# Performance work log

Hardware: AMD Instinct MI355X
Metric: run time of the kernel (lower is better)

The kernel has to match this reference:

```python
import jax, jax.numpy as jnp
import numpy as np

N, L, D, H, DFF = 16, 192, 512, 8, 2048
HD = D // H


def _mha(q, k, v, wq, bq, wk, bk, wv, bv, wo, bo, mask=None):
    # q: [B, Lq, D], k/v: [B, Lk, D]
    B, Lq, _ = q.shape
    def proj(x, W, b):
        y = x @ W + b
        return y.reshape(B, -1, H, HD).transpose(0, 2, 1, 3)  # [B, H, L, HD]
    Q, K, V = proj(q, wq, bq), proj(k, wk, bk), proj(v, wv, bv)
    QK = jnp.einsum('bhqd,bhkd->bhqk', Q, K) / jnp.sqrt(jnp.asarray(HD, Q.dtype))
    if mask is not None:
        QK = QK + (1.0 - mask) * (-1e9)
    A = jax.nn.softmax(QK, axis=-1)
    out = jnp.einsum('bhqk,bhkd->bhqd', A, V).transpose(0, 2, 1, 3).reshape(B, Lq, D)
    return out @ wo + bo


def _ln(x, g, b, eps=1e-6):
    mu = x.mean(-1, keepdims=True)
    var = ((x - mu) ** 2).mean(-1, keepdims=True)
    return (x - mu) / jnp.sqrt(var + eps) * g + b


def setup_inputs() -> dict:
    key = jax.random.key(0)
    ks = jax.random.split(key, 16)
    w = lambda k, sh: jax.random.normal(k, sh, jnp.float32) * 0.02
    inp = {
        'S': jax.random.normal(ks[0], (N, L, D), jnp.float32),
        'padding_mask': jax.random.randint(ks[1], (N * N, 1, 1, L), 0, 2, dtype=jnp.int32),
        'training': 0,
    }
    for i, nm in enumerate(['ca_wq', 'ca_wk', 'ca_wv', 'ca_wo', 'ia_wq', 'ia_wk', 'ia_wv', 'ia_wo']):
        inp[nm] = w(ks[2 + i], (D, D))
        inp[nm.replace('w', 'b')] = jnp.zeros((D,), jnp.float32)
    inp['ffn_w1'] = w(ks[10], (D, DFF)); inp['ffn_b1'] = jnp.zeros((DFF,), jnp.float32)
    inp['ffn_w2'] = w(ks[11], (DFF, D)); inp['ffn_b2'] = jnp.zeros((D,), jnp.float32)
    inp['ln1_g'] = jnp.ones((D,), jnp.float32); inp['ln1_b'] = jnp.zeros((D,), jnp.float32)
    inp['ln2_g'] = jnp.ones((D,), jnp.float32); inp['ln2_b'] = jnp.zeros((D,), jnp.float32)
    return inp


def reference(S, ca_wq, ca_bq, ca_wk, ca_bk, ca_wv, ca_bv, ca_wo, ca_bo,
              ia_wq, ia_bq, ia_wk, ia_bk, ia_wv, ia_bv, ia_wo, ia_bo,
              ffn_w1, ffn_b1, ffn_w2, ffn_b2, ln1_g, ln1_b, ln2_g, ln2_b,
              padding_mask, training):
    # training == 0 -> dropout layers are identity (inference mode)
    mask = padding_mask.astype(S.dtype)
    n, l, d = S.shape
    # all-pairs cross attention: query seq i attends to key/value seq j
    queries = jnp.repeat(S, n, axis=0)   # [n*n, l, d]
    keyvalue = jnp.tile(S, (n, 1, 1))    # [n*n, l, d]
    S_attn = _mha(queries, keyvalue, keyvalue,
                  ca_wq, ca_bq, ca_wk, ca_bk, ca_wv, ca_bv, ca_wo, ca_bo, mask=mask)
    S_attn = S_attn.reshape(n, n, l, d).transpose(1, 2, 0, 3).reshape(n * l, n, d)
    S_flip = S.reshape(n * l, 1, d)
    S_attn = _mha(S_flip, S_attn, S_attn,
                  ia_wq, ia_bq, ia_wk, ia_bk, ia_wv, ia_bv, ia_wo, ia_bo)
    S_attn = S_attn.reshape(n, l, d)
    S_norm = _ln(S + S_attn, ln1_g, ln1_b)
    S_ffn = jax.nn.relu(S_norm @ ffn_w1 + ffn_b1) @ ffn_w2 + ffn_b2
    return _ln(S_norm + S_ffn, ln2_g, ln2_b)
```

## Files before the change

### kernel.cpp

```cpp
#include <hip/hip_runtime.h>


using u16 = unsigned short;
using u32 = unsigned int;
typedef __attribute__((ext_vector_type(8))) short short8;
typedef __attribute__((ext_vector_type(4))) float f32x4;

__device__ __forceinline__ u32 cvtpk(float lo, float hi) {
  u32 r;
  asm("v_cvt_pk_bf16_f32 %0, %1, %2" : "=v"(r) : "v"(lo), "v"(hi));
  return r;
}
__device__ __forceinline__ u16 f2bf(float f) { return (u16)cvtpk(f, f); }
__device__ __forceinline__ float bf2f(u16 h) {
  return __uint_as_float(((u32)h) << 16);
}
__device__ __forceinline__ f32x4 mfma16(short8 a, short8 b, f32x4 c) {
  return __builtin_amdgcn_mfma_f32_16x16x32_bf16(a, b, c, 0, 0, 0);
}
__device__ __forceinline__ void gload16(const void* g, u16* l) {
  __builtin_amdgcn_global_load_lds(
      (const __attribute__((address_space(1))) void*)g,
      (__attribute__((address_space(3))) void*)l, 16, 0, 0);
}

template<int ROWS, int NT>
__device__ __forceinline__ void stage_g16(u16* lds, const u16* __restrict__ src,
                                          int ld, int tid) {
  constexpr int UNITS = ROWS * 8;
  constexpr int WV = NT / 64;
  int lane = tid & 63, w = tid >> 6;
  #pragma unroll
  for (int u = 0; u < UNITS / NT; ++u) {
    int base = (u * WV + w) * 64;
    int unit = base + lane;
    int row = unit >> 3, co = unit & 7;
    gload16(src + (long)row * ld + ((co ^ (row & 7)) << 3), lds + base * 8);
  }
}
template<int ROWS, int NT>
__device__ __forceinline__ void stage_f32(u16* lds, const float* __restrict__ src,
                                          int ld, int tid) {
  constexpr int UNITS = ROWS * 8;
  #pragma unroll
  for (int u = 0; u < UNITS / NT; ++u) {
    int unit = tid + u * NT;
    int row = unit >> 3, co = unit & 7;
    const float* g = src + (long)row * ld + (co << 3);
    float4 a = *(const float4*)g;
    float4 b = *(const float4*)(g + 4);
    u32 p[4] = {cvtpk(a.x, a.y), cvtpk(a.z, a.w),
                cvtpk(b.x, b.y), cvtpk(b.z, b.w)};
    *(uint4*)&lds[(row << 6) + ((co ^ (row & 7)) << 3)] = *(const uint4*)p;
  }
}

template<typename AT, typename BT, int BM, int BN, int WM, int WN>
__device__ __forceinline__ void gemm_core(const AT* __restrict__ A, int lda,
                                          const BT* __restrict__ Bt, int ldb, int K,
                                          u16* As, u16* Bs,
                                          f32x4 (&acc)[BM / (WM * 16)][BN / (WN * 16)]) {
  constexpr int NT = WM * WN * 64;
  constexpr int MI = BM / (WM * 16), NJ = BN / (WN * 16);
  int tid = threadIdx.x, lane = tid & 63, wid = tid >> 6;
  int wr = wid % WM, wc = wid / WM;
  int g = lane >> 4, c = lane & 15;
  #pragma unroll
  for (int mi = 0; mi < MI; ++mi)
    #pragma unroll
    for (int nj = 0; nj < NJ; ++nj)
      acc[mi][nj] = f32x4{0.f, 0.f, 0.f, 0.f};
  for (int kb = 0; kb < K; kb += 64) {
    __syncthreads();
    if constexpr (sizeof(AT) == 4) stage_f32<BM, NT>(As, A + kb, lda, tid);
    else                           stage_g16<BM, NT>(As, A + kb, lda, tid);
    if constexpr (sizeof(BT) == 4) stage_f32<BN, NT>(Bs, Bt + kb, ldb, tid);
    else                           stage_g16<BN, NT>(Bs, Bt + kb, ldb, tid);
    __syncthreads();
    #pragma unroll
    for (int kk = 0; kk < 2; ++kk) {
      int sl = ((kk * 4 + g) ^ (c & 7)) << 3;
      short8 af[MI], bfr[NJ];
      #pragma unroll
      for (int mi = 0; mi < MI; ++mi)
        af[mi] = *(const short8*)&As[((wr * (BM / WM) + mi * 16 + c) << 6) + sl];
      #pragma unroll
      for (int nj = 0; nj < NJ; ++nj)
        bfr[nj] = *(const short8*)&Bs[((wc * (BN / WN) + nj * 16 + c) << 6) + sl];
      #pragma unroll
      for (int mi = 0; mi < MI; ++mi)
        #pragma unroll
        for (int nj = 0; nj < NJ; ++nj)
          acc[mi][nj] = mfma16(af[mi], bfr[nj], acc[mi][nj]);
    }
  }
}

__global__ __launch_bounds__(256) void k_cast(const float* __restrict__ S,
                                              u16* __restrict__ Sb) {
  int idx = (blockIdx.x * 256 + threadIdx.x) * 8;
  float4 a = *(const float4*)(S + idx);
  float4 b = *(const float4*)(S + idx + 4);
  u32 p[4] = {cvtpk(a.x, a.y), cvtpk(a.z, a.w),
              cvtpk(b.x, b.y), cvtpk(b.z, b.w)};
  *(uint4*)(Sb + idx) = *(const uint4*)p;
}

struct TJob { const float* src; u16* dst; int R, C, tile0; };
struct TJobs { TJob j[9]; };

__global__ __launch_bounds__(256) void k_transpose(TJobs jobs) {
  __shared__ float tile[32][33];
  int t = blockIdx.x;
  int ji = 0;
  #pragma unroll
  for (int k = 1; k < 9; ++k)
    if (t >= jobs.j[k].tile0) ji = k;
  TJob jb = jobs.j[ji];
  int lt = t - jb.tile0;
  int tpr = jb.C >> 5;
  int tr = lt / tpr, tc = lt % tpr;
  int tid = threadIdx.x;
  #pragma unroll
  for (int u = 0; u < 4; ++u) {
    int e = tid + u * 256;
    int r = e >> 5, cc = e & 31;
    tile[r][cc] = jb.src[(long)(tr * 32 + r) * jb.C + tc * 32 + cc];
  }
  __syncthreads();
  #pragma unroll
  for (int u = 0; u < 4; ++u) {
    int e = tid + u * 256;
    int r = e >> 5, cc = e & 31;
    jb.dst[(long)(tc * 32 + r) * jb.R + tr * 32 + cc] = f2bf(tile[cc][r]);
  }
}

__global__ __launch_bounds__(256) void k_qkv(const u16* __restrict__ Sb,
    const u16* __restrict__ btAll,
    const float* __restrict__ b0, const float* __restrict__ b1,
    const float* __restrict__ b2, const float* __restrict__ b3,
    u16* __restrict__ Qc, u16* __restrict__ Kc, u16* __restrict__ Vt,
    u16* __restrict__ Qi) {
  __shared__ u16 SH[16384];
  int f = blockIdx.x;
  int swz = (f & 7) * 48 + (f >> 3);
  int mb = swz >> 4, nb = swz & 15;
  f32x4 acc[4][4];
  gemm_core<u16, u16, 128, 128, 2, 2>(Sb + (long)mb * 128 * 512, 512,
                                      btAll + (long)nb * 128 * 512, 512, 512,
                                      SH, SH + 8192, acc);
  int z = nb >> 2;
  const float* bias = z == 0 ? b0 : z == 1 ? b1 : z == 2 ? b2 : b3;
  float scale = (z == 0 || z == 3) ? 0.125f : 1.0f;
  int lane = threadIdx.x & 63, wid = threadIdx.x >> 6;
  int wr = wid & 1, wc = wid >> 1, g = lane >> 4, cl = lane & 15;
  #pragma unroll
  for (int mi = 0; mi < 4; ++mi)
    #pragma unroll
    for (int nj = 0; nj < 4; ++nj)
      #pragma unroll
      for (int r = 0; r < 4; ++r) {
        int row = mb * 128 + wr * 64 + mi * 16 + g * 4 + r;
        int cz = (nb & 3) * 128 + wc * 64 + nj * 16 + cl;
        float v = (acc[mi][nj][r] + bias[cz]) * scale;
        int seq = row / 192, t = row % 192, h = cz >> 6, hd = cz & 63;
        if (z == 0)      Qc[((long)(seq * 8 + h) * 192 + t) * 64 + hd] = f2bf(v);
        else if (z == 1) Kc[((long)(seq * 8 + h) * 192 + t) * 64 + hd] = f2bf(v);
        else if (z == 2) Vt[((long)(seq * 8 + h) * 64 + hd) * 192 + t] = f2bf(v);
        else             Qi[(long)row * 512 + cz] = f2bf(v);
      }
}

__global__ __launch_bounds__(256) void k_attn_up(const u16* __restrict__ Qc,
    const u16* __restrict__ Kc, const u16* __restrict__ VtG,
    const int* __restrict__ mask, u16* __restrict__ AC,
    const u16* __restrict__ Qi, const float* __restrict__ wk,
    u16* __restrict__ U, int attnBlocks) {
  __shared__ __align__(16) u16 SH[24960];
  int bid = blockIdx.x;
  int tid = threadIdx.x, lane = tid & 63, w = tid >> 6;
  int g = lane >> 4, c = lane & 15;
  if (bid < attnBlocks) {
    u16* Ks = SH;
    u16* Vs = SH + 12288;
    float* mbf = (float*)(SH + 24576);
    int b = bid >> 3, h = bid & 7;
    int i = b >> 4, j = b & 15;
    int qb = w * 48;

    const u16* Kbase = Kc + (long)(j * 8 + h) * 192 * 64;
    #pragma unroll
    for (int u = 0; u < 6; ++u) {
      int base = (u * 4 + w) * 64;
      int unit = base + lane;
      int row = unit >> 3, co = unit & 7;
      gload16(Kbase + (long)row * 64 + ((co ^ (row & 7)) << 3), Ks + base * 8);
    }
    const u16* Vbase = VtG + (long)(j * 8 + h) * 64 * 192;
    #pragma unroll
    for (int u = 0; u < 6; ++u) {
      int base = (u * 4 + w) * 64;
      int unit = base + lane;
      int row = unit / 24, co = unit - row * 24;
      gload16(Vbase + (long)row * 192 + ((co ^ (row & 7)) << 3), Vs + base * 8);
    }
    short8 bq[3][2];
    const u16* Qbase = Qc + (long)(i * 8 + h) * 192 * 64;
    #pragma unroll
    for (int nj = 0; nj < 3; ++nj)
      #pragma unroll
      for (int ks = 0; ks < 2; ++ks)
        bq[nj][ks] = *(const short8*)(Qbase + (long)(qb + nj * 16 + c) * 64 + ks * 32 + g * 8);
    if (tid < 192) mbf[tid] = mask[(long)b * 192 + tid] ? 0.f : -1e9f;
    __syncthreads();

    f32x4 oa[4][3];
    #pragma unroll
    for (int mi = 0; mi < 4; ++mi)
      #pragma unroll
      for (int nj = 0; nj < 3; ++nj)
        oa[mi][nj] = f32x4{0.f, 0.f, 0.f, 0.f};
    float sm[3] = {0.f, 0.f, 0.f};
    int srcLo = c | ((g & 1) << 5);
    int srcHi = srcLo + 16;
    int hi = g & 2;

    for (int s = 0; s < 6; ++s) {
      short8 ak[2][2];
      #pragma unroll
      for (int kh = 0; kh < 2; ++kh) {
        int row = (2 * s + kh) * 16 + c;
        #pragma unroll
        for (int ks = 0; ks < 2; ++ks)
          ak[kh][ks] = *(const short8*)&Ks[(row << 6) + (((ks * 4 + g) ^ (c & 7)) << 3)];
      }
      f32x4 sa[2][3];
      __builtin_amdgcn_s_setprio(1);
      #pragma unroll
      for (int kh = 0; kh < 2; ++kh)
        #pragma unroll
        for (int nj = 0; nj < 3; ++nj) {
          sa[kh][nj] = mfma16(ak[kh][0], bq[nj][0], f32x4{0.f, 0.f, 0.f, 0.f});
          sa[kh][nj] = mfma16(ak[kh][1], bq[nj][1], sa[kh][nj]);
        }
      __builtin_amdgcn_s_setprio(0);
      u32 pk[2][3][2];
      #pragma unroll
      for (int kh = 0; kh < 2; ++kh) {
        f32x4 m4 = *(const f32x4*)&mbf[(2 * s + kh) * 16 + g * 4];
        #pragma unroll
        for (int nj = 0; nj < 3; ++nj) {
          float p0 = __expf(sa[kh][nj][0] + m4[0]);
          float p1 = __expf(sa[kh][nj][1] + m4[1]);
          float p2 = __expf(sa[kh][nj][2] + m4[2]);
          float p3 = __expf(sa[kh][nj][3] + m4[3]);
          sm[nj] += (p0 + p1) + (p2 + p3);
          pk[kh][nj][0] = cvtpk(p0, p1);
          pk[kh][nj][1] = cvtpk(p2, p3);
        }
      }
      short8 bfg[3];
      #pragma unroll
      for (int nj = 0; nj < 3; ++nj) {
        u32 w0a = (u32)__shfl((int)pk[0][nj][0], srcLo);
        u32 w0b = (u32)__shfl((int)pk[1][nj][0], srcLo);
        u32 w1a = (u32)__shfl((int)pk[0][nj][1], srcLo);
        u32 w1b = (u32)__shfl((int)pk[1][nj][1], srcLo);
        u32 w2a = (u32)__shfl((int)pk[0][nj][0], srcHi);
        u32 w2b = (u32)__shfl((int)pk[1][nj][0], srcHi);
        u32 w3a = (u32)__shfl((int)pk[0][nj][1], srcHi);
        u32 w3b = (u32)__shfl((int)pk[1][nj][1], srcHi);
        union { u32 u[4]; short8 s8; } bf;
        bf.u[0] = hi ? w0b : w0a;
        bf.u[1] = hi ? w1b : w1a;
        bf.u[2] = hi ? w2b : w2a;
        bf.u[3] = hi ? w3b : w3a;
        bfg[nj] = bf.s8;
      }
      int sl = ((s * 4 + g) ^ (c & 7)) << 3;
      __builtin_amdgcn_s_setprio(1);
      #pragma unroll
      for (int mi = 0; mi < 4; ++mi) {
        short8 av = *(const short8*)&Vs[(mi * 16 + c) * 192 + sl];
        #pragma unroll
        for (int nj = 0; nj < 3; ++nj)
          oa[mi][nj] = mfma16(av, bfg[nj], oa[mi][nj]);
      }
      __builtin_amdgcn_s_setprio(0);
    }
    #pragma unroll
    for (int nj = 0; nj < 3; ++nj) {
      sm[nj] += __shfl_xor(sm[nj], 16);
      sm[nj] += __shfl_xor(sm[nj], 32);
    }
    #pragma unroll
    for (int nj = 0; nj < 3; ++nj) {
      float rs = 1.0f / sm[nj];
      int q = qb + nj * 16 + c;
      u16* dst = AC + ((long)(b * 192 + q)) * 512 + h * 64 + g * 4;
      #pragma unroll
      for (int mi = 0; mi < 4; ++mi) {
        u32 p2[2] = {cvtpk(oa[mi][nj][0] * rs, oa[mi][nj][1] * rs),
                     cvtpk(oa[mi][nj][2] * rs, oa[mi][nj][3] * rs)};
        *(uint2*)(dst + mi * 16) = *(const uint2*)p2;
      }
    }
  } else {
    u16* As = SH;
    u16* Bs = SH + 8192;
    int t = bid - attnBlocks;
    int mb = t % 24, r2 = t / 24;
    int nb = r2 & 3, h = r2 >> 2;
    f32x4 acc[4][4];
    gemm_core<u16, float, 128, 128, 2, 2>(Qi + (long)mb * 128 * 512 + h * 64, 512,
                                          wk + (long)nb * 128 * 512 + h * 64, 512, 64,
                                          As, Bs, acc);
    int wr = w & 1, wc = w >> 1, cl = lane & 15;
    #pragma unroll
    for (int mi = 0; mi < 4; ++mi)
      #pragma unroll
      for (int nj = 0; nj < 4; ++nj)
        #pragma unroll
        for (int r = 0; r < 4; ++r) {
          int row = mb * 128 + wr * 64 + mi * 16 + g * 4 + r;
          int col = nb * 128 + wc * 64 + nj * 16 + cl;
          U[((long)row * 8 + h) * 512 + col] = f2bf(acc[mi][nj][r]);
        }
  }
}

__global__ __launch_bounds__(256) void k_oproj_ca(const u16* __restrict__ AC,
    const u16* __restrict__ woT, const float* __restrict__ bo,
    u16* __restrict__ S2) {
  __shared__ u16 As[128 * 64];
  __shared__ u16 Bs[128 * 64];
  int f = blockIdx.x;
  int swz = (f & 7) * 192 + (f >> 3);
  int mb = swz >> 2, nb = swz & 3;
  f32x4 acc[4][4];
  gemm_core<u16, u16, 128, 128, 2, 2>(AC + (long)mb * 128 * 512, 512,
                                      woT + (long)nb * 128 * 512, 512, 512,
                                      As, Bs, acc);
  int lane = threadIdx.x & 63, wid = threadIdx.x >> 6;
  int wr = wid & 1, wc = wid >> 1, g = lane >> 4, cl = lane & 15;
  #pragma unroll
  for (int mi = 0; mi < 4; ++mi)
    #pragma unroll
    for (int nj = 0; nj < 4; ++nj)
      #pragma unroll
      for (int r = 0; r < 4; ++r) {
        int row = mb * 128 + wr * 64 + mi * 16 + g * 4 + r;
        int col = nb * 128 + wc * 64 + nj * 16 + cl;
        S2[(long)row * 512 + col] = f2bf(acc[mi][nj][r] + bo[col]);
      }
}

__global__ __launch_bounds__(256) void k_ia_attn(const u16* __restrict__ S2,
    const u16* __restrict__ U, const u16* __restrict__ Qi,
    const float* __restrict__ bk, u16* __restrict__ Y) {
  __shared__ u16 s2[16 * 520];
  __shared__ float Lp[4][16][17];
  __shared__ float aL[8][16];
  __shared__ float cL[8];
  int tok = blockIdx.x;
  int tid = threadIdx.x, lane = tid & 63, w = tid >> 6;
  {
    const u16* src = S2 + (long)tok * 512;
    #pragma unroll
    for (int u = 0; u < 4; ++u) {
      int e = tid + u * 256;
      int r = e >> 6, cc = (e & 63) << 3;
      *(uint4*)&s2[r * 520 + cc] = *(const uint4*)(src + (long)r * 3072 * 512 + cc);
    }
  }
  if (w == 0) {
    int h = lane >> 3, p = lane & 7;
    short8 qv = *(const short8*)(Qi + (long)tok * 512 + h * 64 + p * 8);
    const float* bkp = bk + h * 64 + p * 8;
    float s = 0.f;
    #pragma unroll
    for (int v = 0; v < 8; ++v) s += bf2f((u16)qv[v]) * bkp[v];
    s += __shfl_xor(s, 1); s += __shfl_xor(s, 2); s += __shfl_xor(s, 4);
    if (p == 0) cL[h] = s;
  }
  __syncthreads();
  {
    int g = lane >> 4, c = lane & 15;
    const u16* Ub = U + (long)tok * 4096 + (long)(c & 7) * 512;
    f32x4 accL = {0.f, 0.f, 0.f, 0.f};
    #pragma unroll
    for (int kk = 0; kk < 4; ++kk) {
      int d = w * 128 + kk * 32 + g * 8;
      short8 aS = *(const short8*)&s2[c * 520 + d];
      short8 bU = *(const short8*)(Ub + d);
      accL = mfma16(aS, bU, accL);
    }
    #pragma unroll
    for (int r = 0; r < 4; ++r) Lp[w][g * 4 + r][c] = accL[r];
  }
  __syncthreads();
  if (w == 0) {
    int h = lane & 7, i0 = lane >> 3;
    float L0 = Lp[0][i0][h] + Lp[1][i0][h] + Lp[2][i0][h] + Lp[3][i0][h] + cL[h];
    float L1 = Lp[0][i0 + 8][h] + Lp[1][i0 + 8][h] + Lp[2][i0 + 8][h] +
               Lp[3][i0 + 8][h] + cL[h];
    float e0 = __expf(L0), e1 = __expf(L1);
    float s = e0 + e1;
    s += __shfl_xor(s, 8); s += __shfl_xor(s, 16); s += __shfl_xor(s, 32);
    float rs = 1.0f / s;
    aL[h][i0] = e0 * rs;
    aL[h][i0 + 8] = e1 * rs;
  }
  __syncthreads();
  {
    int h = tid & 7, d0 = (tid >> 3) << 4;
    float y[16];
    #pragma unroll
    for (int v = 0; v < 16; ++v) y[v] = 0.f;
    #pragma unroll
    for (int i = 0; i < 16; ++i) {
      float a = aL[h][i];
      short8 v0 = *(const short8*)&s2[i * 520 + d0];
      short8 v1 = *(const short8*)&s2[i * 520 + d0 + 8];
      #pragma unroll
      for (int v = 0; v < 8; ++v) {
        y[v]     += a * bf2f((u16)v0[v]);
        y[8 + v] += a * bf2f((u16)v1[v]);
      }
    }
    u32 o[8];
    #pragma unroll
    for (int v = 0; v < 8; ++v) o[v] = cvtpk(y[2 * v], y[2 * v + 1]);
    u16* dst = Y + ((long)tok * 8 + h) * 512 + d0;
    *(uint4*)dst = *(const uint4*)&o[0];
    *(uint4*)(dst + 8) = *(const uint4*)&o[4];
  }
}

__global__ __launch_bounds__(256) void k_vapply(const u16* __restrict__ Y,
    const u16* __restrict__ wvT, const float* __restrict__ bv,
    u16* __restrict__ AO) {
  __shared__ u16 As[128 * 64];
  __shared__ u16 Bs[64 * 64];
  int mb = blockIdx.x, h = blockIdx.z;
  f32x4 acc[2][4];
  gemm_core<u16, u16, 128, 64, 4, 1>(Y + (long)mb * 128 * 4096 + h * 512, 4096,
                                     wvT + (long)h * 64 * 512, 512, 512,
                                     As, Bs, acc);
  int lane = threadIdx.x & 63, wid = threadIdx.x >> 6;
  int g = lane >> 4, cl = lane & 15;
  #pragma unroll
  for (int mi = 0; mi < 2; ++mi)
    #pragma unroll
    for (int nj = 0; nj < 4; ++nj)
      #pragma unroll
      for (int r = 0; r < 4; ++r) {
        int row = mb * 128 + wid * 32 + mi * 16 + g * 4 + r;
        int col = h * 64 + nj * 16 + cl;
        AO[(long)row * 512 + col] = f2bf(acc[mi][nj][r] + bv[col]);
      }
}

__global__ __launch_bounds__(256) void k_gemm_f32out(const u16* __restrict__ A, int K,
    const u16* __restrict__ BT, const float* __restrict__ bias,
    float* __restrict__ out) {
  __shared__ u16 As[128 * 64];
  __shared__ u16 Bs[64 * 64];
  int f = blockIdx.x;
  int swz = (f & 7) * 24 + (f >> 3);
  int mb = swz >> 3, nb = swz & 7;
  f32x4 acc[4][2];
  gemm_core<u16, u16, 128, 64, 2, 2>(A + (long)mb * 128 * K, K,
                                     BT + (long)nb * 64 * K, K, K, As, Bs, acc);
  int lane = threadIdx.x & 63, wid = threadIdx.x >> 6;
  int wr = wid & 1, wc = wid >> 1, g = lane >> 4, cl = lane & 15;
  #pragma unroll
  for (int mi = 0; mi < 4; ++mi)
    #pragma unroll
    for (int nj = 0; nj < 2; ++nj)
      #pragma unroll
      for (int r = 0; r < 4; ++r) {
        int row = mb * 128 + wr * 64 + mi * 16 + g * 4 + r;
        int col = nb * 64 + wc * 32 + nj * 16 + cl;
        out[(long)row * 512 + col] = acc[mi][nj][r] + bias[col];
      }
}

__global__ __launch_bounds__(256) void k_ffn1(const u16* __restrict__ A,
    const u16* __restrict__ BT, const float* __restrict__ bias,
    u16* __restrict__ out) {
  __shared__ u16 As[128 * 64];
  __shared__ u16 Bs[128 * 64];
  int f = blockIdx.x;
  int swz = (f & 7) * 48 + (f >> 3);
  int mb = swz >> 4, nb = swz & 15;
  f32x4 acc[4][4];
  gemm_core<u16, u16, 128, 128, 2, 2>(A + (long)mb * 128 * 512, 512,
                                      BT + (long)nb * 128 * 512, 512, 512,
                                      As, Bs, acc);
  int lane = threadIdx.x & 63, wid = threadIdx.x >> 6;
  int wr = wid & 1, wc = wid >> 1, g = lane >> 4, cl = lane & 15;
  #pragma unroll
  for (int mi = 0; mi < 4; ++mi)
    #pragma unroll
    for (int nj = 0; nj < 4; ++nj)
      #pragma unroll
      for (int r = 0; r < 4; ++r) {
        int row = mb * 128 + wr * 64 + mi * 16 + g * 4 + r;
        int col = nb * 128 + wc * 64 + nj * 16 + cl;
        out[(long)row * 2048 + col] = f2bf(fmaxf(acc[mi][nj][r] + bias[col], 0.f));
      }
}

__global__ __launch_bounds__(256) void k_ln(const float* __restrict__ X1,
    const float* __restrict__ X2, const float* __restrict__ gg,
    const float* __restrict__ bb, float* __restrict__ outF,
    u16* __restrict__ outB) {
  __shared__ float red[8];
  int row = blockIdx.x, tid = threadIdx.x;
  long base = (long)row * 512;
  float x0 = X1[base + tid] + X2[base + tid];
  float x1 = X1[base + tid + 256] + X2[base + tid + 256];
  float s = x0 + x1, ss = x0 * x0 + x1 * x1;
  #pragma unroll
  for (int m = 1; m <= 32; m <<= 1) {
    s += __shfl_xor(s, m);
    ss += __shfl_xor(ss, m);
  }
  int w = tid >> 6;
  if ((tid & 63) == 0) { red[w] = s; red[4 + w] = ss; }
  __syncthreads();
  s = red[0] + red[1] + red[2] + red[3];
  ss = red[4] + red[5] + red[6] + red[7];
  float mu = s * (1.0f / 512.0f);
  float var = ss * (1.0f / 512.0f) - mu * mu;
  float rstd = 1.0f / sqrtf(var + 1e-6f);
  float y0 = (x0 - mu) * rstd * gg[tid] + bb[tid];
  float y1 = (x1 - mu) * rstd * gg[tid + 256] + bb[tid + 256];
  if (outF) { outF[base + tid] = y0; outF[base + tid + 256] = y1; }
  if (outB) { outB[base + tid] = f2bf(y0); outB[base + tid + 256] = f2bf(y1); }
}

extern "C" void kernel_launch(void* const* d_in, const int* in_sizes, int n_in,
                              void* d_out, int out_size, void* d_ws, size_t ws_size,
                              hipStream_t stream) {
  const float* S      = (const float*)d_in[0];
  const int*   maskp  = (const int*)d_in[1];
  const float* ca_wq  = (const float*)d_in[3];
  const float* ca_bq  = (const float*)d_in[4];
  const float* ca_wk  = (const float*)d_in[5];
  const float* ca_bk  = (const float*)d_in[6];
  const float* ca_wv  = (const float*)d_in[7];
  const float* ca_bv  = (const float*)d_in[8];
  const float* ca_wo  = (const float*)d_in[9];
  const float* ca_bo  = (const float*)d_in[10];
  const float* ia_wq  = (const float*)d_in[11];
  const float* ia_bq  = (const float*)d_in[12];
  const float* ia_wk  = (const float*)d_in[13];
  const float* ia_bk  = (const float*)d_in[14];
  const float* ia_wv  = (const float*)d_in[15];
  const float* ia_bv  = (const float*)d_in[16];
  const float* ia_wo  = (const float*)d_in[17];
  const float* ia_bo  = (const float*)d_in[18];
  const float* ffn_w1 = (const float*)d_in[19];
  const float* ffn_b1 = (const float*)d_in[20];
  const float* ffn_w2 = (const float*)d_in[21];
  const float* ffn_b2 = (const float*)d_in[22];
  const float* ln1_g  = (const float*)d_in[23];
  const float* ln1_b  = (const float*)d_in[24];
  const float* ln2_g  = (const float*)d_in[25];
  const float* ln2_b  = (const float*)d_in[26];

  char* ws = (char*)d_ws;
  constexpr size_t OFF_WQT  = 0;
  constexpr size_t OFF_WOTC = 2097152;
  constexpr size_t OFF_WVTI = 2621440;
  constexpr size_t OFF_WOTI = 3145728;
  constexpr size_t OFF_W1T  = 3670016;
  constexpr size_t OFF_W2T  = 5767168;
  constexpr size_t OFF_QC   = 7864320;
  constexpr size_t OFF_KC   = 11010048;
  constexpr size_t OFF_VT   = 14155776;
  constexpr size_t OFF_QI   = 17301504;
  constexpr size_t OFF_AC   = 20447232;
  constexpr size_t OFF_S2   = 70778880;
  constexpr size_t OFF_UBIG = 121110528;
  constexpr size_t NEED_BIG = OFF_UBIG + 25165824;
  constexpr size_t OFF_SB   = OFF_AC;
  constexpr size_t OFF_Y    = OFF_AC + 25165824;
  constexpr size_t OFF_AO   = OFF_QI;
  constexpr size_t OFF_IAO  = OFF_QC;
  constexpr size_t OFF_SNB  = OFF_VT;
  constexpr size_t OFF_SNF  = OFF_S2;
  constexpr size_t OFF_HFF  = OFF_S2 + 6291456;
  constexpr size_t OFF_FFO  = OFF_HFF + 12582912;

  u16* wqT  = (u16*)(ws + OFF_WQT);
  u16* woTc = (u16*)(ws + OFF_WOTC);
  u16* wvTi = (u16*)(ws + OFF_WVTI);
  u16* woTi = (u16*)(ws + OFF_WOTI);
  u16* w1T  = (u16*)(ws + OFF_W1T);
  u16* w2T  = (u16*)(ws + OFF_W2T);
  u16* Qc   = (u16*)(ws + OFF_QC);
  u16* Kc   = (u16*)(ws + OFF_KC);
  u16* Vt   = (u16*)(ws + OFF_VT);
  u16* Qi   = (u16*)(ws + OFF_QI);
  u16* AC   = (u16*)(ws + OFF_AC);
  u16* Sb   = (u16*)(ws + OFF_SB);
  u16* S2   = (u16*)(ws + OFF_S2);
  u16* Y    = (u16*)(ws + OFF_Y);
  u16* AO   = (u16*)(ws + OFF_AO);
  float* IAO = (float*)(ws + OFF_IAO);
  u16* SNB  = (u16*)(ws + OFF_SNB);
  float* SNF = (float*)(ws + OFF_SNF);
  u16* HFF  = (u16*)(ws + OFF_HFF);
  float* FFO = (float*)(ws + OFF_FFO);

  bool bigws = ws_size >= NEED_BIG;
  u16* U = bigws ? (u16*)(ws + OFF_UBIG) : (u16*)(ws + OFF_AC);

  TJobs tj;
  int t0 = 0;
  auto SET = [&](int k, const float* s, u16* d, int R, int C) {
    tj.j[k].src = s; tj.j[k].dst = d; tj.j[k].R = R; tj.j[k].C = C; tj.j[k].tile0 = t0;
    t0 += (R / 32) * (C / 32);
  };
  SET(0, ca_wq, wqT, 512, 512);
  SET(1, ca_wk, wqT + 262144, 512, 512);
  SET(2, ca_wv, wqT + 524288, 512, 512);
  SET(3, ia_wq, wqT + 786432, 512, 512);
  SET(4, ca_wo, woTc, 512, 512);
  SET(5, ia_wv, wvTi, 512, 512);
  SET(6, ia_wo, woTi, 512, 512);
  SET(7, ffn_w1, w1T, 512, 2048);
  SET(8, ffn_w2, w2T, 2048, 512);

  k_cast<<<dim3(768), 256, 0, stream>>>(S, Sb);
  k_transpose<<<dim3(t0), 256, 0, stream>>>(tj);
  k_qkv<<<dim3(384), 256, 0, stream>>>(Sb, wqT, ca_bq, ca_bk, ca_bv, ia_bq,
                                       Qc, Kc, Vt, Qi);
  if (bigws) {
    k_attn_up<<<dim3(2816), 256, 0, stream>>>(Qc, Kc, Vt, maskp, AC, Qi, ia_wk,
                                              U, 2048);
    k_oproj_ca<<<dim3(1536), 256, 0, stream>>>(AC, woTc, ca_bo, S2);
  } else {
    k_attn_up<<<dim3(2048), 256, 0, stream>>>(Qc, Kc, Vt, maskp, AC, Qi, ia_wk,
                                              U, 2048);
    k_oproj_ca<<<dim3(1536), 256, 0, stream>>>(AC, woTc, ca_bo, S2);
    k_attn_up<<<dim3(768), 256, 0, stream>>>(Qc, Kc, Vt, maskp, AC, Qi, ia_wk,
                                             U, 0);
  }
  k_ia_attn<<<dim3(3072), 256, 0, stream>>>(S2, U, Qi, ia_bk, Y);
  k_vapply<<<dim3(24, 1, 8), 256, 0, stream>>>(Y, wvTi, ia_bv, AO);
  k_gemm_f32out<<<dim3(192), 256, 0, stream>>>(AO, 512, woTi, ia_bo, IAO);
  k_ln<<<dim3(3072), 256, 0, stream>>>(S, IAO, ln1_g, ln1_b, SNF, SNB);
  k_ffn1<<<dim3(384), 256, 0, stream>>>(SNB, w1T, ffn_b1, HFF);
  k_gemm_f32out<<<dim3(192), 256, 0, stream>>>(HFF, 2048, w2T, ffn_b2, FFO);
  k_ln<<<dim3(3072), 256, 0, stream>>>(SNF, FFO, ln2_g, ln2_b, (float*)d_out, nullptr);
}
```

Before: 209.5 us.

## Replace cross-attention output projection with 256x256 tile, 8-wave double-buffered GEMM

Replaces the 128x128 tile output-projection GEMM with a 256x256 tile kernel using 512 threads and 128KB of dynamic LDS. Tiles are double-buffered through direct global-to-LDS loads, and MFMA phases are interleaved with LDS fragment reads and prefetches, coordinated by barriers and priority hints. The aim is more operand reuse per load and better overlap of memory with compute, at the cost of one block per CU and fewer blocks overall. It also adds a partial unroll to the attention score loop.

```diff
diff --git a/kernel.cpp b/kernel.cpp
--- a/kernel.cpp
+++ b/kernel.cpp
@@ -226,6 +226,7 @@
     int srcHi = srcLo + 16;
     int hi = g & 2;
 
+    #pragma unroll 2
     for (int s = 0; s < 6; ++s) {
       short8 ak[2][2];
       #pragma unroll
@@ -330,30 +331,144 @@
   }
 }
 
-__global__ __launch_bounds__(256) void k_oproj_ca(const u16* __restrict__ AC,
+__global__ __launch_bounds__(512, 1) void k_oproj8(const u16* __restrict__ AC,
     const u16* __restrict__ woT, const float* __restrict__ bo,
     u16* __restrict__ S2) {
-  __shared__ u16 As[128 * 64];
-  __shared__ u16 Bs[128 * 64];
+  extern __shared__ u16 LDS[];
   int f = blockIdx.x;
-  int swz = (f & 7) * 192 + (f >> 3);
-  int mb = swz >> 2, nb = swz & 3;
-  f32x4 acc[4][4];
-  gemm_core<u16, u16, 128, 128, 2, 2>(AC + (long)mb * 128 * 512, 512,
-                                      woT + (long)nb * 128 * 512, 512, 512,
-                                      As, Bs, acc);
-  int lane = threadIdx.x & 63, wid = threadIdx.x >> 6;
-  int wr = wid & 1, wc = wid >> 1, g = lane >> 4, cl = lane & 15;
-  #pragma unroll
-  for (int mi = 0; mi < 4; ++mi)
+  int swz = (f & 7) * 48 + (f >> 3);
+  int mb = swz >> 1, nb = swz & 1;
+  int tid = threadIdx.x, lane = tid & 63, wid = tid >> 6;
+  int wr = wid >> 2, wc = wid & 3;
+  int g = lane >> 4, c = lane & 15;
+  const u16* Abase = AC + (long)mb * 256 * 512;
+  const u16* Bbase = woT + (long)nb * 256 * 512;
+
+  auto STAGE = [&](int opOff, int buf, int half, int kt, const u16* base) {
+    u16* ldst = LDS + opOff + buf * 16384 + half * 8192;
+    const u16* gsrc = base + (long)half * 128 * 512 + kt * 64;
+    #pragma unroll
+    for (int u = 0; u < 2; ++u) {
+      int unit = tid + u * 512;
+      int row = unit >> 3, co = unit & 7;
+      gload16(gsrc + (long)row * 512 + ((co ^ (row & 7)) << 3), ldst + unit * 8);
+    }
+  };
+
+  f32x4 acc[8][4];
+  #pragma unroll
+  for (int mi = 0; mi < 8; ++mi)
     #pragma unroll
     for (int nj = 0; nj < 4; ++nj)
+      acc[mi][nj] = f32x4{0.f, 0.f, 0.f, 0.f};
+
+  STAGE(0, 0, 0, 0, Abase);     STAGE(0, 0, 1, 0, Abase);
+  STAGE(32768, 0, 0, 0, Bbase); STAGE(32768, 0, 1, 0, Bbase);
+  STAGE(0, 1, 0, 1, Abase);     STAGE(0, 1, 1, 1, Abase);
+  STAGE(32768, 1, 0, 1, Bbase); STAGE(32768, 1, 1, 1, Bbase);
+  asm volatile("s_waitcnt vmcnt(8)");
+  __builtin_amdgcn_s_barrier();
+
+  short8 aLo[8], aHi[8], bLo[4], bHi[4];
+  for (int t = 0; t < 8; ++t) {
+    int buf = t & 1;
+    int abase = buf * 16384, bbase = 32768 + buf * 16384;
+    #pragma unroll
+    for (int m = 0; m < 4; ++m)
+      #pragma unroll
+      for (int kk = 0; kk < 2; ++kk)
+        aLo[m * 2 + kk] = *(const short8*)&LDS[abase +
+            (wr * 128 + m * 16 + c) * 64 + (((kk * 4 + g) ^ (c & 7)) << 3)];
+    #pragma unroll
+    for (int n = 0; n < 2; ++n)
+      #pragma unroll
+      for (int kk = 0; kk < 2; ++kk)
+        bLo[n * 2 + kk] = *(const short8*)&LDS[bbase +
+            (wc * 64 + n * 16 + c) * 64 + (((kk * 4 + g) ^ (c & 7)) << 3)];
+    __builtin_amdgcn_s_barrier();
+    asm volatile("s_waitcnt lgkmcnt(0)");
+    __builtin_amdgcn_sched_barrier(0);
+    __builtin_amdgcn_s_setprio(1);
+    #pragma unroll
+    for (int m = 0; m < 4; ++m)
+      #pragma unroll
+      for (int n = 0; n < 2; ++n)
+        #pragma unroll
+        for (int kk = 0; kk < 2; ++kk)
+          acc[m][n] = mfma16(aLo[m * 2 + kk], bLo[n * 2 + kk], acc[m][n]);
+    __builtin_amdgcn_s_setprio(0);
+    __builtin_amdgcn_s_barrier();
+    #pragma unroll
+    for (int m = 0; m < 4; ++m)
+      #pragma unroll
+      for (int kk = 0; kk < 2; ++kk)
+        aHi[m * 2 + kk] = *(const short8*)&LDS[abase +
+            (wr * 128 + (4 + m) * 16 + c) * 64 + (((kk * 4 + g) ^ (c & 7)) << 3)];
+    __builtin_amdgcn_s_barrier();
+    asm volatile("s_waitcnt lgkmcnt(0)");
+    __builtin_amdgcn_sched_barrier(0);
+    __builtin_amdgcn_s_setprio(1);
+    #pragma unroll
+    for (int m = 0; m < 4; ++m)
+      #pragma unroll
+      for (int n = 0; n < 2; ++n)
+        #pragma unroll
+        for (int kk = 0; kk < 2; ++kk)
+          acc[4 + m][n] = mfma16(aHi[m * 2 + kk], bLo[n * 2 + kk], acc[4 + m][n]);
+    __builtin_amdgcn_s_setprio(0);
+    __builtin_amdgcn_s_barrier();
+    #pragma unroll
+    for (int n = 0; n < 2; ++n)
+      #pragma unroll
+      for (int kk = 0; kk < 2; ++kk)
+        bHi[n * 2 + kk] = *(const short8*)&LDS[bbase +
+            (wc * 64 + (2 + n) * 16 + c) * 64 + (((kk * 4 + g) ^ (c & 7)) << 3)];
+    if (t < 6) {
+      STAGE(0, buf, 0, t + 2, Abase);
+      STAGE(0, buf, 1, t + 2, Abase);
+    }
+    __builtin_amdgcn_s_barrier();
+    asm volatile("s_waitcnt lgkmcnt(0)");
+    __builtin_amdgcn_sched_barrier(0);
+    __builtin_amdgcn_s_setprio(1);
+    #pragma unroll
+    for (int m = 0; m < 4; ++m)
+      #pragma unroll
+      for (int n = 0; n < 2; ++n)
+        #pragma unroll
+        for (int kk = 0; kk < 2; ++kk)
+          acc[m][2 + n] = mfma16(aLo[m * 2 + kk], bHi[n * 2 + kk], acc[m][2 + n]);
+    __builtin_amdgcn_s_setprio(0);
+    __builtin_amdgcn_s_barrier();
+    if (t < 6) {
+      STAGE(32768, buf, 0, t + 2, Bbase);
+      STAGE(32768, buf, 1, t + 2, Bbase);
+    }
+    __builtin_amdgcn_s_setprio(1);
+    #pragma unroll
+    for (int m = 0; m < 4; ++m)
+      #pragma unroll
+      for (int n = 0; n < 2; ++n)
+        #pragma unroll
+        for (int kk = 0; kk < 2; ++kk)
+          acc[4 + m][2 + n] = mfma16(aHi[m * 2 + kk], bHi[n * 2 + kk], acc[4 + m][2 + n]);
+    __builtin_amdgcn_s_setprio(0);
+    if (t < 6)      asm volatile("s_waitcnt vmcnt(8)");
+    else if (t == 6) asm volatile("s_waitcnt vmcnt(0)");
+    if (t < 7) __builtin_amdgcn_s_barrier();
+  }
+  #pragma unroll
+  for (int nj = 0; nj < 4; ++nj) {
+    int col = nb * 256 + wc * 64 + nj * 16 + c;
+    float bv = bo[col];
+    #pragma unroll
+    for (int mi = 0; mi < 8; ++mi)
       #pragma unroll
       for (int r = 0; r < 4; ++r) {
-        int row = mb * 128 + wr * 64 + mi * 16 + g * 4 + r;
-        int col = nb * 128 + wc * 64 + nj * 16 + cl;
-        S2[(long)row * 512 + col] = f2bf(acc[mi][nj][r] + bo[col]);
-      }
+        int row = mb * 256 + wr * 128 + mi * 16 + g * 4 + r;
+        S2[(long)row * 512 + col] = f2bf(acc[mi][nj][r] + bv);
+      }
+  }
 }
 
 __global__ __launch_bounds__(256) void k_ia_attn(const u16* __restrict__ S2,
@@ -620,6 +735,13 @@
   bool bigws = ws_size >= NEED_BIG;
   u16* U = bigws ? (u16*)(ws + OFF_UBIG) : (u16*)(ws + OFF_AC);
 
+  static bool attrDone = false;
+  if (!attrDone) {
+    (void)hipFuncSetAttribute(reinterpret_cast<const void*>(&k_oproj8),
+                              hipFuncAttributeMaxDynamicSharedMemorySize, 131072);
+    attrDone = true;
+  }
+
   TJobs tj;
   int t0 = 0;
   auto SET = [&](int k, const float* s, u16* d, int R, int C) {
@@ -643,11 +765,11 @@
   if (bigws) {
     k_attn_up<<<dim3(2816), 256, 0, stream>>>(Qc, Kc, Vt, maskp, AC, Qi, ia_wk,
                                               U, 2048);
-    k_oproj_ca<<<dim3(1536), 256, 0, stream>>>(AC, woTc, ca_bo, S2);
+    k_oproj8<<<dim3(384), 512, 131072, stream>>>(AC, woTc, ca_bo, S2);
   } else {
     k_attn_up<<<dim3(2048), 256, 0, stream>>>(Qc, Kc, Vt, maskp, AC, Qi, ia_wk,
                                               U, 2048);
-    k_oproj_ca<<<dim3(1536), 256, 0, stream>>>(AC, woTc, ca_bo, S2);
+    k_oproj8<<<dim3(384), 512, 131072, stream>>>(AC, woTc, ca_bo, S2);
     k_attn_up<<<dim3(768), 256, 0, stream>>>(Qc, Kc, Vt, maskp, AC, Qi, ia_wk,
                                              U, 0);
   }
```

Result: slower. 220.9 us (+5.5%).
